# Kernel tuning notes

Measured on AMD Instinct MI355X. Metric: run time of the kernel, lower is better.

Reference implementation:

```python
import jax, jax.numpy as jnp
import numpy as np

T, OBS, H, NOBJ = 32768, 256, 512, 4


def _xavier(key, shape):
    fan_in, fan_out = shape[0], shape[1]
    lim = jnp.sqrt(6.0 / (fan_in + fan_out)).astype(jnp.float32)
    return jax.random.uniform(key, shape, jnp.float32, -lim, lim)


def setup_inputs() -> dict:
    key = jax.random.key(0)
    ks = jax.random.split(key, 16)
    # weights stored as [in, out] so y = x @ W (same math as nn.Linear with W.T)
    return {
        "x": jax.random.normal(ks[0], (T, OBS), jnp.float32),
        "W_in0": _xavier(ks[1], (OBS, H)),
        "W_B0": _xavier(ks[2], (OBS, H)),
        "W_C0": _xavier(ks[3], (OBS, H)),
        "W_d0": _xavier(ks[4], (OBS, H)),
        "A_log0": jax.random.normal(ks[5], (H,), jnp.float32),
        "W_in1": _xavier(ks[6], (H, H)),
        "W_B1": _xavier(ks[7], (H, H)),
        "W_C1": _xavier(ks[8], (H, H)),
        "W_d1": _xavier(ks[9], (H, H)),
        "A_log1": jax.random.normal(ks[10], (H,), jnp.float32),
        "W_out": _xavier(ks[11], (H, NOBJ)),
        "b_out": jnp.zeros((NOBJ,), jnp.float32),
        "W_skip": _xavier(ks[12], (OBS, NOBJ)),
    }


def _mamba_layer(x, W_in, W_B, W_C, W_d, A_log):
    # x: [T, D_in] -> [T, H]
    x_state = x @ W_in           # [T, H]
    B = x @ W_B                  # [T, H]
    C = x @ W_C                  # [T, H]
    delta = jax.nn.sigmoid(x @ W_d)  # [T, H]
    A = -jnp.exp(A_log)          # [H]
    A_bar = jnp.exp(delta * A)   # [T, H], in (0, 1)
    Bx = B * x_state             # [T, H]

    def step(h, inp):
        a_t, bx_t = inp
        h = a_t * h + bx_t
        return h, h

    h0 = jnp.zeros((x_state.shape[-1],), x_state.dtype)
    _, h_seq = jax.lax.scan(step, h0, (A_bar, Bx))  # [T, H]
    return C * h_seq


def reference(x, W_in0, W_B0, W_C0, W_d0, A_log0,
              W_in1, W_B1, W_C1, W_d1, A_log1,
              W_out, b_out, W_skip):
    skip = x
    y = _mamba_layer(x, W_in0, W_B0, W_C0, W_d0, A_log0)
    y = _mamba_layer(y, W_in1, W_B1, W_C1, W_d1, A_log1)
    out = y @ W_out + b_out + skip @ W_skip  # [T, NOBJ]
    return out
```

## Files before the change

kernel.cpp:

```cpp
#include <hip/hip_runtime.h>

typedef __attribute__((ext_vector_type(8))) short short8;
typedef __attribute__((ext_vector_type(4))) float floatx4;

#define T_SIZE 32768
#define OBS    256
#define H      512
#define NC     1024
#define CHUNK  32
#define NGRP   64
#define GCH    16

__device__ __forceinline__ unsigned short f2bf(float f){
    union { float f; unsigned u; } v; v.f = f;
    unsigned u = v.u;
    u += 0x7FFFu + ((u >> 16) & 1u);
    return (unsigned short)(u >> 16);
}
__device__ __forceinline__ float bf2f(unsigned short u){
    union { unsigned u; float f; } v; v.u = ((unsigned)u) << 16; return v.f;
}

#define GLOAD_LDS16(g, l) \
    __builtin_amdgcn_global_load_lds((const __attribute__((address_space(1))) unsigned*)(g), \
                                     (__attribute__((address_space(3))) unsigned*)(l), 16, 0, 0)

__global__ void prep_kernel(const float* __restrict__ x, unsigned short* __restrict__ xb,
                            const float* __restrict__ A0W0, const float* __restrict__ A0W1,
                            const float* __restrict__ A0W2, const float* __restrict__ A0W3,
                            unsigned short* __restrict__ Wt0,
                            const float* __restrict__ A1W0, const float* __restrict__ A1W1,
                            const float* __restrict__ A1W2, const float* __restrict__ A1W3,
                            unsigned short* __restrict__ Wt1){
    const int b = blockIdx.x;
    const int tid = threadIdx.x;
    if (b < 8192){
        int i = b * 256 + tid;
        float4 v = ((const float4*)x)[i];
        ushort4 o;
        o.x = f2bf(v.x); o.y = f2bf(v.y); o.z = f2bf(v.z); o.w = f2bf(v.w);
        ((ushort4*)xb)[i] = o;
    } else if (b < 10240){
        const int K = OBS, KH = OBS * H;
        int idx = (b - 8192) * 256 + tid;
        int s   = idx / KH;
        int rem = idx - s * KH;
        int k = rem >> 9;
        int h = rem & 511;
        const float* W = (s == 0) ? A0W0 : (s == 1) ? A0W1 : (s == 2) ? A0W2 : A0W3;
        int bb = h >> 4, hh = h & 15;
        Wt0[(size_t)((bb * 4 + s) * 16 + hh) * K + k] = f2bf(W[(size_t)k * H + h]);
    } else {
        const int K = H, KH = H * H;
        int idx = (b - 10240) * 256 + tid;
        int s   = idx / KH;
        int rem = idx - s * KH;
        int k = rem >> 9;
        int h = rem & 511;
        const float* W = (s == 0) ? A1W0 : (s == 1) ? A1W1 : (s == 2) ? A1W2 : A1W3;
        int bb = h >> 4, hh = h & 15;
        Wt1[(size_t)((bb * 4 + s) * 16 + hh) * K + k] = f2bf(W[(size_t)k * H + h]);
    }
}

template<int K>
__global__ __launch_bounds__(256) void gemm_layer_kernel(
    const unsigned short* __restrict__ xb,
    const unsigned short* __restrict__ wt,
    const float* __restrict__ A_log,
    unsigned short* __restrict__ gT, unsigned short* __restrict__ bxT, unsigned short* __restrict__ CT,
    float* __restrict__ Pbuf, float* __restrict__ Hbuf)
{
    __shared__ unsigned short SM[4][8192];

    const int tid  = threadIdx.x;
    const int wave = tid >> 6;
    const int lane = tid & 63;
    const int ml   = lane & 15;
    const int quad = lane >> 4;
    const int wm   = wave & 1;
    const int wn   = wave >> 1;

    const int flat = blockIdx.y * 16 + blockIdx.x;
    const int xcd  = flat & 7;
    const int j    = flat >> 3;
    const int nb   = j & 15;
    const int mb   = (j >> 4) * 8 + xcd;
    const int m0   = mb * 128;

    const int srow = tid >> 2;
    const int sel  = (((tid & 3) ^ ((tid >> 3) & 3))) * 8;
    const int swz  = (ml >> 1) & 3;

    const unsigned short* pa0 = xb + (size_t)(m0 + srow) * K + sel;
    const unsigned short* pa1 = pa0 + (size_t)64 * K;
    const unsigned short* pb0 = wt + (size_t)(nb * 128 + srow) * K + sel;
    const unsigned short* pb1 = pb0 + (size_t)64 * K;

    const int ldsA0 = (wave * 64 + 0  ) * 8;
    const int ldsA1 = (wave * 64 + 256) * 8;

    const int rbaseA = (wm * 64 + ml) * 32 + (quad ^ swz) * 8;
    const int rbaseB = (wn * 64 + ml) * 32 + (quad ^ swz) * 8;

    floatx4 acc[4][4];
    #pragma unroll
    for (int i = 0; i < 4; i++)
        #pragma unroll
        for (int jj = 0; jj < 4; jj++)
            acc[i][jj] = (floatx4)(0.0f);

    constexpr int NK = K >> 5;

    #pragma unroll
    for (int p = 0; p < 3; ++p){
        const int ko = p * 32;
        GLOAD_LDS16(pa0 + ko, &SM[p][ldsA0]);
        GLOAD_LDS16(pa1 + ko, &SM[p][ldsA1]);
        GLOAD_LDS16(pb0 + ko, &SM[p][4096 + ldsA0]);
        GLOAD_LDS16(pb1 + ko, &SM[p][4096 + ldsA1]);
    }
    asm volatile("s_waitcnt vmcnt(8)" ::: "memory");
    __builtin_amdgcn_s_barrier();
    __builtin_amdgcn_sched_barrier(0);

    #pragma unroll
    for (int kk = 0; kk < NK; ++kk){
        const int cur = kk & 3;

        if (kk + 3 < NK){
            const int ko  = (kk + 3) * 32;
            const int nb4 = (kk + 3) & 3;
            GLOAD_LDS16(pa0 + ko, &SM[nb4][ldsA0]);
            GLOAD_LDS16(pa1 + ko, &SM[nb4][ldsA1]);
            GLOAD_LDS16(pb0 + ko, &SM[nb4][4096 + ldsA0]);
            GLOAD_LDS16(pb1 + ko, &SM[nb4][4096 + ldsA1]);
        }

        short8 av[4], bv[4];
        #pragma unroll
        for (int i = 0; i < 4; i++)
            av[i] = *(const short8*)(&SM[cur][0] + rbaseA + i * 16 * 32);
        #pragma unroll
        for (int jj = 0; jj < 4; jj++)
            bv[jj] = *(const short8*)(&SM[cur][4096] + rbaseB + jj * 16 * 32);

        __builtin_amdgcn_s_setprio(1);
        #pragma unroll
        for (int i = 0; i < 4; i++)
            #pragma unroll
            for (int jj = 0; jj < 4; jj++)
                acc[i][jj] = __builtin_amdgcn_mfma_f32_16x16x32_bf16(av[i], bv[jj], acc[i][jj], 0, 0, 0);
        __builtin_amdgcn_s_setprio(0);

        if (kk + 1 < NK){
            const int hi = (kk + 3 < NK) ? (kk + 3) : (NK - 1);
            const int vm = 4 * (hi - (kk + 1));
            if (vm >= 8)      asm volatile("s_waitcnt vmcnt(8)" ::: "memory");
            else if (vm == 4) asm volatile("s_waitcnt vmcnt(4)" ::: "memory");
            else              asm volatile("s_waitcnt vmcnt(0)" ::: "memory");
            __builtin_amdgcn_s_barrier();
            __builtin_amdgcn_sched_barrier(0);
        }
    }
    __syncthreads();

    unsigned short* SMe = &SM[0][0];
    float2* segbuf = (float2*)(SMe + 12288);
    const int col = wn * 16 + ml;
    const int h   = nb * 32 + col;
    const float Aneg = -expf(A_log[h]);

    #pragma unroll
    for (int i = 0; i < 4; i++){
        float p = 1.0f, hh = 0.0f;
        #pragma unroll
        for (int r = 0; r < 4; r++){
            int trow = wm * 64 + i * 16 + quad * 4 + r;
            float dv = acc[i][3][r];
            float delta = 1.0f / (1.0f + expf(-dv));
            unsigned short gb = f2bf(delta * Aneg);
            float a = expf(bf2f(gb));
            unsigned short bb = f2bf(acc[i][1][r] * acc[i][0][r]);
            SMe[        trow * 32 + col] = gb;
            SMe[4096 +  trow * 32 + col] = bb;
            SMe[8192 +  trow * 32 + col] = f2bf(acc[i][2][r]);
            hh = fmaf(a, hh, bf2f(bb));
            p *= a;
        }
        const int ch = wm * 2 + (i >> 1);
        const int s  = (i & 1) * 4 + quad;
        segbuf[(ch * 8 + s) * 32 + col] = make_float2(p, hh);
    }
    __syncthreads();
    {
        const short8* s8 = (const short8*)SMe;
        #pragma unroll
        for (int arr = 0; arr < 3; arr++){
            unsigned short* bp = (arr == 0) ? gT : (arr == 1) ? bxT : CT;
            #pragma unroll
            for (int half = 0; half < 2; half++){
                int u = half * 256 + tid;
                int row = u >> 2, part = u & 3;
                *(short8*)(bp + (size_t)(m0 + row) * H + nb * 32 + part * 8) = s8[arr * 512 + u];
            }
        }
    }
    if (tid < 128){
        const int ccol = tid & 31, ch = tid >> 5;
        float P = 1.0f, Hc = 0.0f;
        #pragma unroll
        for (int s = 0; s < 8; s++){
            float2 ph = segbuf[(ch * 8 + s) * 32 + ccol];
            Hc = fmaf(ph.x, Hc, ph.y);
            P *= ph.x;
        }
        const int c = mb * 4 + ch;
        Pbuf[(size_t)c * H + nb * 32 + ccol] = P;
        Hbuf[(size_t)c * H + nb * 32 + ccol] = Hc;
    }
}

__global__ void scan2a_kernel(const float* __restrict__ P, const float* __restrict__ Hc,
                              float* __restrict__ Pg, float* __restrict__ Hg){
    const int g  = blockIdx.x;
    const int j4 = threadIdx.x * 4;
    float4 pc = {1.f,1.f,1.f,1.f}, hc = {0.f,0.f,0.f,0.f};
    #pragma unroll
    for (int i = 0; i < GCH; i++){
        size_t o = (size_t)(g * GCH + i) * H + j4;
        float4 P4 = *(const float4*)(P + o);
        float4 H4 = *(const float4*)(Hc + o);
        hc.x = fmaf(P4.x, hc.x, H4.x); pc.x *= P4.x;
        hc.y = fmaf(P4.y, hc.y, H4.y); pc.y *= P4.y;
        hc.z = fmaf(P4.z, hc.z, H4.z); pc.z *= P4.z;
        hc.w = fmaf(P4.w, hc.w, H4.w); pc.w *= P4.w;
    }
    *(float4*)(Pg + (size_t)g * H + j4) = pc;
    *(float4*)(Hg + (size_t)g * H + j4) = hc;
}

__global__ void scan3_kernel(const unsigned short* __restrict__ gT, const unsigned short* __restrict__ bxT,
                             const unsigned short* __restrict__ CT,
                             const float* __restrict__ P, const float* __restrict__ Hc,
                             const float* __restrict__ Pg, const float* __restrict__ Hg,
                             unsigned short* __restrict__ yb){
    int idx = blockIdx.x * 256 + threadIdx.x;
    int j4 = (idx & 127) * 4;
    int c  = idx >> 7;
    int grp = c >> 4;
    float4 h = {0.f, 0.f, 0.f, 0.f};
    for (int g = 0; g < grp; ++g){
        float4 P4 = *(const float4*)(Pg + (size_t)g * H + j4);
        float4 H4 = *(const float4*)(Hg + (size_t)g * H + j4);
        h.x = fmaf(P4.x, h.x, H4.x);
        h.y = fmaf(P4.y, h.y, H4.y);
        h.z = fmaf(P4.z, h.z, H4.z);
        h.w = fmaf(P4.w, h.w, H4.w);
    }
    for (int cc = grp << 4; cc < c; ++cc){
        float4 P4 = *(const float4*)(P + (size_t)cc * H + j4);
        float4 H4 = *(const float4*)(Hc + (size_t)cc * H + j4);
        h.x = fmaf(P4.x, h.x, H4.x);
        h.y = fmaf(P4.y, h.y, H4.y);
        h.z = fmaf(P4.z, h.z, H4.z);
        h.w = fmaf(P4.w, h.w, H4.w);
    }
    size_t off = (size_t)c * CHUNK * H + j4;
    #pragma unroll 8
    for (int i = 0; i < CHUNK; i++){
        ushort4 gv = *(const ushort4*)(gT + off);
        ushort4 bv = *(const ushort4*)(bxT + off);
        ushort4 cv = *(const ushort4*)(CT + off);
        h.x = fmaf(expf(bf2f(gv.x)), h.x, bf2f(bv.x));
        h.y = fmaf(expf(bf2f(gv.y)), h.y, bf2f(bv.y));
        h.z = fmaf(expf(bf2f(gv.z)), h.z, bf2f(bv.z));
        h.w = fmaf(expf(bf2f(gv.w)), h.w, bf2f(bv.w));
        ushort4 o;
        o.x = f2bf(bf2f(cv.x) * h.x);
        o.y = f2bf(bf2f(cv.y) * h.y);
        o.z = f2bf(bf2f(cv.z) * h.z);
        o.w = f2bf(bf2f(cv.w) * h.w);
        *(ushort4*)(yb + off) = o;
        off += H;
    }
}

__global__ __launch_bounds__(256) void scan3f_kernel(
    const unsigned short* __restrict__ gT, const unsigned short* __restrict__ bxT,
    const unsigned short* __restrict__ CT,
    const float* __restrict__ P, const float* __restrict__ Hc,
    const float* __restrict__ Pg, const float* __restrict__ Hg,
    const unsigned short* __restrict__ xb,
    const float* __restrict__ Wout, const float* __restrict__ bout,
    const float* __restrict__ Wskip,
    float* __restrict__ out){
    __shared__ unsigned short ystage[64 * 512];
    const int tid = threadIdx.x;
    int idx = blockIdx.x * 256 + tid;
    int j4 = (idx & 127) * 4;
    int c  = idx >> 7;
    int grp = c >> 4;
    float4 h = {0.f, 0.f, 0.f, 0.f};
    for (int g = 0; g < grp; ++g){
        float4 P4 = *(const float4*)(Pg + (size_t)g * H + j4);
        float4 H4 = *(const float4*)(Hg + (size_t)g * H + j4);
        h.x = fmaf(P4.x, h.x, H4.x);
        h.y = fmaf(P4.y, h.y, H4.y);
        h.z = fmaf(P4.z, h.z, H4.z);
        h.w = fmaf(P4.w, h.w, H4.w);
    }
    for (int cc = grp << 4; cc < c; ++cc){
        float4 P4 = *(const float4*)(P + (size_t)cc * H + j4);
        float4 H4 = *(const float4*)(Hc + (size_t)cc * H + j4);
        h.x = fmaf(P4.x, h.x, H4.x);
        h.y = fmaf(P4.y, h.y, H4.y);
        h.z = fmaf(P4.z, h.z, H4.z);
        h.w = fmaf(P4.w, h.w, H4.w);
    }
    size_t off = (size_t)c * CHUNK * H + j4;
    const int lrow = (tid >> 7) * 32;
    #pragma unroll 8
    for (int i = 0; i < CHUNK; i++){
        ushort4 gv = *(const ushort4*)(gT + off);
        ushort4 bv = *(const ushort4*)(bxT + off);
        ushort4 cv = *(const ushort4*)(CT + off);
        h.x = fmaf(expf(bf2f(gv.x)), h.x, bf2f(bv.x));
        h.y = fmaf(expf(bf2f(gv.y)), h.y, bf2f(bv.y));
        h.z = fmaf(expf(bf2f(gv.z)), h.z, bf2f(bv.z));
        h.w = fmaf(expf(bf2f(gv.w)), h.w, bf2f(bv.w));
        ushort4 o;
        o.x = f2bf(bf2f(cv.x) * h.x);
        o.y = f2bf(bf2f(cv.y) * h.y);
        o.z = f2bf(bf2f(cv.z) * h.z);
        o.w = f2bf(bf2f(cv.w) * h.w);
        *(ushort4*)(&ystage[(lrow + i) * 512 + j4]) = o;
        off += H;
    }
    __syncthreads();

    const int wave = tid >> 6;
    const int lane = tid & 63;
    const float4* W4 = (const float4*)Wout;
    const float4* S4 = (const float4*)Wskip;
    const float b0 = bout[0], b1 = bout[1], b2 = bout[2], b3 = bout[3];
    for (int rr = 0; rr < 16; ++rr){
        const int r = wave * 16 + rr;
        const int t = blockIdx.x * 64 + r;
        float s0 = 0.f, s1 = 0.f, s2 = 0.f, s3 = 0.f;
        #pragma unroll
        for (int k = lane; k < H; k += 64){
            float yv = bf2f(ystage[r * 512 + k]);
            float4 w = W4[k];
            s0 = fmaf(yv, w.x, s0); s1 = fmaf(yv, w.y, s1);
            s2 = fmaf(yv, w.z, s2); s3 = fmaf(yv, w.w, s3);
        }
        #pragma unroll
        for (int k = lane; k < OBS; k += 64){
            float xv = bf2f(xb[(size_t)t * OBS + k]);
            float4 w = S4[k];
            s0 = fmaf(xv, w.x, s0); s1 = fmaf(xv, w.y, s1);
            s2 = fmaf(xv, w.z, s2); s3 = fmaf(xv, w.w, s3);
        }
        #pragma unroll
        for (int o = 32; o > 0; o >>= 1){
            s0 += __shfl_down(s0, o);
            s1 += __shfl_down(s1, o);
            s2 += __shfl_down(s2, o);
            s3 += __shfl_down(s3, o);
        }
        if (lane == 0){
            out[(size_t)t * 4 + 0] = s0 + b0;
            out[(size_t)t * 4 + 1] = s1 + b1;
            out[(size_t)t * 4 + 2] = s2 + b2;
            out[(size_t)t * 4 + 3] = s3 + b3;
        }
    }
}

extern "C" void kernel_launch(void* const* d_in, const int* in_sizes, int n_in,
                              void* d_out, int out_size, void* d_ws, size_t ws_size,
                              hipStream_t stream)
{
    const float* x     = (const float*)d_in[0];
    const float* W_in0 = (const float*)d_in[1];
    const float* W_B0  = (const float*)d_in[2];
    const float* W_C0  = (const float*)d_in[3];
    const float* W_d0  = (const float*)d_in[4];
    const float* A0    = (const float*)d_in[5];
    const float* W_in1 = (const float*)d_in[6];
    const float* W_B1  = (const float*)d_in[7];
    const float* W_C1  = (const float*)d_in[8];
    const float* W_d1  = (const float*)d_in[9];
    const float* A1    = (const float*)d_in[10];
    const float* Wout  = (const float*)d_in[11];
    const float* bout  = (const float*)d_in[12];
    const float* Wskip = (const float*)d_in[13];
    float* out = (float*)d_out;

    char* ws = (char*)d_ws;
    size_t off = 0;
    auto alloc = [&](size_t bytes) -> void* {
        void* p = ws + off;
        off += (bytes + 255) & ~(size_t)255;
        return p;
    };
    unsigned short* xb  = (unsigned short*)alloc((size_t)T_SIZE * OBS * 2);
    unsigned short* yb  = (unsigned short*)alloc((size_t)T_SIZE * H * 2);
    unsigned short* Wt0 = (unsigned short*)alloc((size_t)4 * H * OBS * 2);
    unsigned short* Wt1 = (unsigned short*)alloc((size_t)4 * H * H * 2);
    unsigned short* gT  = (unsigned short*)alloc((size_t)T_SIZE * H * 2);
    unsigned short* bxT = (unsigned short*)alloc((size_t)T_SIZE * H * 2);
    unsigned short* CT  = (unsigned short*)alloc((size_t)T_SIZE * H * 2);
    float* Pbuf = (float*)alloc((size_t)NC * H * 4);
    float* Hbuf = (float*)alloc((size_t)NC * H * 4);
    float* Pg   = (float*)alloc((size_t)NGRP * H * 4);
    float* Hg   = (float*)alloc((size_t)NGRP * H * 4);
    (void)ws_size; (void)in_sizes; (void)n_in; (void)out_size;

    prep_kernel<<<14336, 256, 0, stream>>>(x, xb,
                                           W_in0, W_B0, W_C0, W_d0, Wt0,
                                           W_in1, W_B1, W_C1, W_d1, Wt1);

    dim3 ggrid(16, 256);
    const int sgrid = NC * 128 / 256;

    gemm_layer_kernel<OBS><<<ggrid, 256, 0, stream>>>(xb, Wt0, A0, gT, bxT, CT, Pbuf, Hbuf);
    scan2a_kernel<<<NGRP, 128, 0, stream>>>(Pbuf, Hbuf, Pg, Hg);
    scan3_kernel<<<sgrid, 256, 0, stream>>>(gT, bxT, CT, Pbuf, Hbuf, Pg, Hg, yb);

    gemm_layer_kernel<H><<<ggrid, 256, 0, stream>>>(yb, Wt1, A1, gT, bxT, CT, Pbuf, Hbuf);
    scan2a_kernel<<<NGRP, 128, 0, stream>>>(Pbuf, Hbuf, Pg, Hg);
    scan3f_kernel<<<sgrid, 256, 0, stream>>>(gT, bxT, CT, Pbuf, Hbuf, Pg, Hg,
                                             xb, Wout, bout, Wskip, out);
}
```

Before: 330.8 us.

## Load pre-swizzled weight fragments directly into registers, bypassing LDS for B

The weight-transpose kernel now writes weights in an MFMA-fragment-friendly blocked layout: groups of 8 consecutive k values per column, packed in 128-element tiles. The GEMM loads B operand fragments straight from global memory into registers with a two-deep register double buffer. Only the A tile is staged through LDS, which halves shared memory and removes the B LDS reads and writes. In exchange, waves that share B columns each fetch the same weights from cache, and the epilogue's LDS scratch must still fit in the smaller array.

```diff
diff --git a/kernel.cpp b/kernel.cpp
--- a/kernel.cpp
+++ b/kernel.cpp
@@ -49,7 +49,8 @@
         int h = rem & 511;
         const float* W = (s == 0) ? A0W0 : (s == 1) ? A0W1 : (s == 2) ? A0W2 : A0W3;
         int bb = h >> 4, hh = h & 15;
-        Wt0[(size_t)((bb * 4 + s) * 16 + hh) * K + k] = f2bf(W[(size_t)k * H + h]);
+        Wt0[((size_t)(bb * 4 + s) * (K >> 3) + (k >> 3)) * 128 + hh * 8 + (k & 7)]
+            = f2bf(W[(size_t)k * H + h]);
     } else {
         const int K = H, KH = H * H;
         int idx = (b - 10240) * 256 + tid;
@@ -59,7 +60,8 @@
         int h = rem & 511;
         const float* W = (s == 0) ? A1W0 : (s == 1) ? A1W1 : (s == 2) ? A1W2 : A1W3;
         int bb = h >> 4, hh = h & 15;
-        Wt1[(size_t)((bb * 4 + s) * 16 + hh) * K + k] = f2bf(W[(size_t)k * H + h]);
+        Wt1[((size_t)(bb * 4 + s) * (K >> 3) + (k >> 3)) * 128 + hh * 8 + (k & 7)]
+            = f2bf(W[(size_t)k * H + h]);
     }
 }
 
@@ -71,7 +73,7 @@
     unsigned short* __restrict__ gT, unsigned short* __restrict__ bxT, unsigned short* __restrict__ CT,
     float* __restrict__ Pbuf, float* __restrict__ Hbuf)
 {
-    __shared__ unsigned short SM[4][8192];
+    __shared__ unsigned short SM[4][4096];
 
     const int tid  = threadIdx.x;
     const int wave = tid >> 6;
@@ -94,14 +96,16 @@
 
     const unsigned short* pa0 = xb + (size_t)(m0 + srow) * K + sel;
     const unsigned short* pa1 = pa0 + (size_t)64 * K;
-    const unsigned short* pb0 = wt + (size_t)(nb * 128 + srow) * K + sel;
-    const unsigned short* pb1 = pb0 + (size_t)64 * K;
-
-    const int ldsA0 = (wave * 64 + 0  ) * 8;
-    const int ldsA1 = (wave * 64 + 256) * 8;
+
+    const unsigned short* pB0 = wt + ((size_t)(nb * 8 + wn * 4 + 0) * (K >> 3) + quad) * 128 + ml * 8;
+    const unsigned short* pB1 = wt + ((size_t)(nb * 8 + wn * 4 + 1) * (K >> 3) + quad) * 128 + ml * 8;
+    const unsigned short* pB2 = wt + ((size_t)(nb * 8 + wn * 4 + 2) * (K >> 3) + quad) * 128 + ml * 8;
+    const unsigned short* pB3 = wt + ((size_t)(nb * 8 + wn * 4 + 3) * (K >> 3) + quad) * 128 + ml * 8;
+
+    const int ldsA0 = wave * 512;
+    const int ldsA1 = 2048 + wave * 512;
 
     const int rbaseA = (wm * 64 + ml) * 32 + (quad ^ swz) * 8;
-    const int rbaseB = (wn * 64 + ml) * 32 + (quad ^ swz) * 8;
 
     floatx4 acc[4][4];
     #pragma unroll
@@ -112,58 +116,56 @@
 
     constexpr int NK = K >> 5;
 
-    #pragma unroll
-    for (int p = 0; p < 3; ++p){
-        const int ko = p * 32;
-        GLOAD_LDS16(pa0 + ko, &SM[p][ldsA0]);
-        GLOAD_LDS16(pa1 + ko, &SM[p][ldsA1]);
-        GLOAD_LDS16(pb0 + ko, &SM[p][4096 + ldsA0]);
-        GLOAD_LDS16(pb1 + ko, &SM[p][4096 + ldsA1]);
-    }
-    asm volatile("s_waitcnt vmcnt(8)" ::: "memory");
+#define STAGE_A(kt_) { const int b_ = (kt_) & 3; const int ko_ = (kt_) * 32; \
+        GLOAD_LDS16(pa0 + ko_, &SM[b_][ldsA0]); \
+        GLOAD_LDS16(pa1 + ko_, &SM[b_][ldsA1]); }
+#define LOADB(BV, kt_) { const size_t o_ = (size_t)(kt_) * 512; \
+        BV[0] = *(const short8*)(pB0 + o_); \
+        BV[1] = *(const short8*)(pB1 + o_); \
+        BV[2] = *(const short8*)(pB2 + o_); \
+        BV[3] = *(const short8*)(pB3 + o_); }
+
+    short8 bvA[4], bvB[4];
+
+    STAGE_A(0); STAGE_A(1); STAGE_A(2);
+    LOADB(bvA, 0); LOADB(bvB, 1);
+    asm volatile("s_waitcnt vmcnt(4)" ::: "memory");
     __builtin_amdgcn_s_barrier();
     __builtin_amdgcn_sched_barrier(0);
 
+#define KSTEP(kk_, BV) { \
+        const int cur_ = (kk_) & 3; \
+        short8 av_[4]; \
+        _Pragma("unroll") \
+        for (int i_ = 0; i_ < 4; i_++) \
+            av_[i_] = *(const short8*)(&SM[cur_][0] + rbaseA + i_ * 512); \
+        if ((kk_) + 3 < NK) STAGE_A((kk_) + 3); \
+        __builtin_amdgcn_s_setprio(1); \
+        _Pragma("unroll") \
+        for (int i_ = 0; i_ < 4; i_++) \
+            _Pragma("unroll") \
+            for (int j_ = 0; j_ < 4; j_++) \
+                acc[i_][j_] = __builtin_amdgcn_mfma_f32_16x16x32_bf16(av_[i_], BV[j_], acc[i_][j_], 0, 0, 0); \
+        __builtin_amdgcn_s_setprio(0); \
+        if ((kk_) + 2 < NK) LOADB(BV, (kk_) + 2); \
+        if ((kk_) + 1 < NK){ \
+            if ((kk_) + 3 < NK)      { asm volatile("s_waitcnt vmcnt(6)" ::: "memory"); } \
+            else if ((kk_) + 2 < NK) { asm volatile("s_waitcnt vmcnt(4)" ::: "memory"); } \
+            else                     { asm volatile("s_waitcnt vmcnt(0)" ::: "memory"); } \
+            __builtin_amdgcn_s_barrier(); \
+            __builtin_amdgcn_sched_barrier(0); \
+        } }
+
     #pragma unroll
-    for (int kk = 0; kk < NK; ++kk){
-        const int cur = kk & 3;
-
-        if (kk + 3 < NK){
-            const int ko  = (kk + 3) * 32;
-            const int nb4 = (kk + 3) & 3;
-            GLOAD_LDS16(pa0 + ko, &SM[nb4][ldsA0]);
-            GLOAD_LDS16(pa1 + ko, &SM[nb4][ldsA1]);
-            GLOAD_LDS16(pb0 + ko, &SM[nb4][4096 + ldsA0]);
-            GLOAD_LDS16(pb1 + ko, &SM[nb4][4096 + ldsA1]);
-        }
-
-        short8 av[4], bv[4];
-        #pragma unroll
-        for (int i = 0; i < 4; i++)
-            av[i] = *(const short8*)(&SM[cur][0] + rbaseA + i * 16 * 32);
-        #pragma unroll
-        for (int jj = 0; jj < 4; jj++)
-            bv[jj] = *(const short8*)(&SM[cur][4096] + rbaseB + jj * 16 * 32);
-
-        __builtin_amdgcn_s_setprio(1);
-        #pragma unroll
-        for (int i = 0; i < 4; i++)
-            #pragma unroll
-            for (int jj = 0; jj < 4; jj++)
-                acc[i][jj] = __builtin_amdgcn_mfma_f32_16x16x32_bf16(av[i], bv[jj], acc[i][jj], 0, 0, 0);
-        __builtin_amdgcn_s_setprio(0);
-
-        if (kk + 1 < NK){
-            const int hi = (kk + 3 < NK) ? (kk + 3) : (NK - 1);
-            const int vm = 4 * (hi - (kk + 1));
-            if (vm >= 8)      asm volatile("s_waitcnt vmcnt(8)" ::: "memory");
-            else if (vm == 4) asm volatile("s_waitcnt vmcnt(4)" ::: "memory");
-            else              asm volatile("s_waitcnt vmcnt(0)" ::: "memory");
-            __builtin_amdgcn_s_barrier();
-            __builtin_amdgcn_sched_barrier(0);
-        }
+    for (int k2 = 0; k2 < NK; k2 += 2){
+        KSTEP(k2,     bvA);
+        KSTEP(k2 + 1, bvB);
     }
     __syncthreads();
+
+#undef KSTEP
+#undef LOADB
+#undef STAGE_A
 
     unsigned short* SMe = &SM[0][0];
     float2* segbuf = (float2*)(SMe + 12288);
```

After: 334.4 us. Within noise of the previous version (+1.1%).
